# Optimization experiments

Hardware: AMD Instinct MI355X
Metric: run time of the kernel (lower is better)

The kernel has to match this reference:

```python
import jax, jax.numpy as jnp
import numpy as np

MAX_ITERS = 256  # matches init_kwargs max_iters


def setup_inputs() -> dict:
    key = jax.random.key(0)
    k1, k2 = jax.random.split(key)
    H = W = 4096
    # classic Mandelbrot viewing window
    c_real = jax.random.uniform(k1, (H, W), jnp.float32, -2.0, 0.5)
    c_imag = jax.random.uniform(k2, (H, W), jnp.float32, -1.25, 1.25)
    return {"c_real": c_real, "c_imag": c_imag}


def reference(c_real, c_imag):
    # z starts at c (NOT zero), as in the torch module
    zr0 = c_real
    zi0 = c_imag
    active0 = jnp.ones(c_real.shape, dtype=bool)
    counts0 = jnp.full(c_real.shape, float(MAX_ITERS), dtype=c_real.dtype)

    def body(step, state):
        zr, zi, active, counts = state
        escaped_now = active & (zr * zr + zi * zi >= 4.0)
        counts = jnp.where(escaped_now, step.astype(counts.dtype), counts)
        active = active & ~escaped_now
        # torch loop only updates z for step < max_iters
        do_update = active & (step < MAX_ITERS)
        next_real = zr * zr - zi * zi + c_real
        next_imag = 2.0 * zr * zi + c_imag
        zr = jnp.where(do_update, next_real, zr)
        zi = jnp.where(do_update, next_imag, zi)
        return (zr, zi, active, counts)

    _, _, _, counts = jax.lax.fori_loop(
        0, MAX_ITERS + 1, body, (zr0, zi0, active0, counts0)
    )
    return counts
```

## Files before the change

kernel.cpp:

```cpp
#include <hip/hip_runtime.h>


#define MAX_ITERS 256

__device__ __forceinline__ float mul32(float a, float b) {
    float d; asm("v_mul_f32 %0, %1, %2" : "=v"(d) : "v"(a), "v"(b)); return d;
}
__device__ __forceinline__ float add32(float a, float b) {
    float d; asm("v_add_f32 %0, %1, %2" : "=v"(d) : "v"(a), "v"(b)); return d;
}
__device__ __forceinline__ float fma32(float a, float b, float c) {
    float d; asm("v_fma_f32 %0, %1, %2, %3" : "=v"(d) : "v"(a), "v"(b), "v"(c)); return d;
}
__device__ __forceinline__ float fma32_negc(float a, float b, float c) {
    float d; asm("v_fma_f32 %0, %1, %2, -%3" : "=v"(d) : "v"(a), "v"(b), "v"(c)); return d;
}

__device__ __forceinline__ void iter_checks(float cr, float ci,
                                            float& zr, float& zi,
                                            float& act, float& cnt, int nchecks)
{
    #pragma unroll 8
    for (int s = 0; s < nchecks; ++s) {
        const float zi2 = mul32(zi, zi);
        const float mag = fma32(zr, zr, zi2);
        act = (mag < 4.0f) ? act : 0.0f;
        cnt = cnt + act;
        const float t   = fma32_negc(zr, zr, zi2);
        const float nr  = add32(t, cr);
        const float t2  = add32(zr, zr);
        zi = fma32(t2, zi, ci);
        zr = nr;
    }
}

__global__ void zero_ctrs(unsigned char* ws) {
    if (threadIdx.x < 64) *(unsigned*)(ws + (size_t)threadIdx.x * 64u) = 0u;
}

__global__ __launch_bounds__(256) void mandel_stage_a(
    const float* __restrict__ c_real, const float* __restrict__ c_imag,
    float* __restrict__ out, unsigned char* __restrict__ ws,
    unsigned seg_cap, int n)
{
    int i = blockIdx.x * blockDim.x + threadIdx.x;
    if (i >= n) return;
    const float cr = c_real[i];
    const float ci = c_imag[i];

    const float xq = cr - 0.25f;
    const float q  = xq * xq + ci * ci;
    const bool in_card = (q * (q + xq) - 0.25f * ci * ci) < -1e-3f;
    const float xb = cr + 1.0f;
    const bool in_bulb = (xb * xb + ci * ci) < (0.0625f - 1e-3f);
    const bool shortcut = in_card | in_bulb;

    float zr = cr, zi = ci, act = 1.0f, cnt = 0.0f;
    iter_checks(cr, ci, zr, zi, act, cnt, 16);

    const bool surv = (!shortcut) && (act != 0.0f);

    const unsigned long long m = __ballot(surv);
    if (m != 0ull) {
        const int lane = __builtin_amdgcn_mbcnt_hi(
            ~0u, __builtin_amdgcn_mbcnt_lo(~0u, 0));
        const int leader = (int)__ffsll((unsigned long long)m) - 1;
        const int seg = blockIdx.x & 63;
        unsigned* ctr = (unsigned*)(ws + (size_t)seg * 64u);
        unsigned base = 0u;
        if (lane == leader) base = atomicAdd(ctr, (unsigned)__popcll(m));
        base = (unsigned)__shfl((int)base, leader, 64);
        if (surv) {
            const unsigned rank = (unsigned)__popcll(m & ((1ull << lane) - 1ull));
            const unsigned slot = base + rank;
            if (slot < seg_cap) {
                float4* q1 = (float4*)(ws + 4096);
                int*    q2 = (int*)(ws + 4096 + (size_t)seg_cap * 64u * 16u);
                const size_t p = (size_t)seg * seg_cap + slot;
                q1[p] = make_float4(zr, zi, cr, ci);
                q2[p] = i;
                return;
            }
            iter_checks(cr, ci, zr, zi, act, cnt, 240);
            out[i] = cnt;
            return;
        }
    }
    out[i] = shortcut ? 256.0f : cnt;
}

__global__ __launch_bounds__(256) void mandel_stage_b(
    float* __restrict__ out, const unsigned char* __restrict__ ws,
    unsigned seg_cap, int blocks_per_seg)
{
    const int seg = (int)(blockIdx.x & 63u);
    const int grp = (int)(blockIdx.x >> 6);
    const unsigned cnt_s = *(const unsigned*)(ws + (size_t)seg * 64u);
    const unsigned nq = (cnt_s < seg_cap) ? cnt_s : seg_cap;
    const float4* q1 = (const float4*)(ws + 4096);
    const int*    q2 = (const int*)(ws + 4096 + (size_t)seg_cap * 64u * 16u);
    const unsigned stride = (unsigned)blocks_per_seg * 256u;
    for (unsigned j = (unsigned)grp * 256u + threadIdx.x; j < nq; j += stride) {
        const size_t p = (size_t)seg * seg_cap + j;
        const float4 rec = q1[p];
        const int idx = q2[p];
        float zr = rec.x, zi = rec.y;
        const float cr = rec.z, ci = rec.w;
        float act = 1.0f, cnt = 16.0f;
        iter_checks(cr, ci, zr, zi, act, cnt, 240);
        out[idx] = cnt;
    }
}

__global__ __launch_bounds__(256) void mandel_mono(
    const float* __restrict__ c_real, const float* __restrict__ c_imag,
    float* __restrict__ out, int n)
{
    int i = blockIdx.x * blockDim.x + threadIdx.x;
    if (i >= n) return;
    const float cr = c_real[i], ci = c_imag[i];
    float zr = cr, zi = ci, act = 1.0f, cnt = 0.0f;
    iter_checks(cr, ci, zr, zi, act, cnt, MAX_ITERS);
    out[i] = cnt;
}

extern "C" void kernel_launch(void* const* d_in, const int* in_sizes, int n_in,
                              void* d_out, int out_size, void* d_ws, size_t ws_size,
                              hipStream_t stream)
{
    const float* c_real = (const float*)d_in[0];
    const float* c_imag = (const float*)d_in[1];
    float* out = (float*)d_out;
    const int n = in_sizes[0];
    const int block = 256;
    const int gridA = (n + block - 1) / block;

    unsigned char* ws = (unsigned char*)d_ws;
    const size_t avail = (ws_size > 4096) ? (ws_size - 4096) : 0;
    unsigned seg_cap = (unsigned)(avail / (64u * 20u));

    if (seg_cap < 1024u) {
        mandel_mono<<<gridA, block, 0, stream>>>(c_real, c_imag, out, n);
        return;
    }

    zero_ctrs<<<1, 64, 0, stream>>>(ws);
    mandel_stage_a<<<gridA, block, 0, stream>>>(c_real, c_imag, out, ws,
                                                seg_cap, n);
    const int blocks_per_seg = 256;
    mandel_stage_b<<<64 * blocks_per_seg, block, 0, stream>>>(out, ws, seg_cap,
                                                              blocks_per_seg);
}
```

Measured before the change: 258.3 us.

## Make stage B persistent with per-lane dynamic refill from segment queues

Stage B changes from a static grid-stride loop, where each thread runs a full 240-iteration check, to a persistent kernel. Each lane works in 12-iteration chunks and, once its pixel escapes or finishes, grabs a new queued pixel through a wave-level atomic cursor per segment. The goal is to cut SIMD divergence waste, where lanes whose pixels escaped early sat idle while slower lanes in the same wavefront finished. In exchange it adds per-chunk ballots, atomics and scattered queue loads, and launches far fewer blocks. The counter-zeroing kernel now also clears the new cursor words.

```diff
diff --git a/kernel.cpp b/kernel.cpp
--- a/kernel.cpp
+++ b/kernel.cpp
@@ -35,7 +35,9 @@
 }
 
 __global__ void zero_ctrs(unsigned char* ws) {
-    if (threadIdx.x < 64) *(unsigned*)(ws + (size_t)threadIdx.x * 64u) = 0u;
+    if (threadIdx.x < 128)
+        *(unsigned*)(ws + (size_t)(threadIdx.x >> 1) * 64u
+                        + (size_t)(threadIdx.x & 1) * 4u) = 0u;
 }
 
 __global__ __launch_bounds__(256) void mandel_stage_a(
@@ -90,25 +92,53 @@
 }
 
 __global__ __launch_bounds__(256) void mandel_stage_b(
-    float* __restrict__ out, const unsigned char* __restrict__ ws,
-    unsigned seg_cap, int blocks_per_seg)
+    float* __restrict__ out, unsigned char* __restrict__ ws,
+    unsigned seg_cap)
 {
     const int seg = (int)(blockIdx.x & 63u);
-    const int grp = (int)(blockIdx.x >> 6);
     const unsigned cnt_s = *(const unsigned*)(ws + (size_t)seg * 64u);
     const unsigned nq = (cnt_s < seg_cap) ? cnt_s : seg_cap;
     const float4* q1 = (const float4*)(ws + 4096);
     const int*    q2 = (const int*)(ws + 4096 + (size_t)seg_cap * 64u * 16u);
-    const unsigned stride = (unsigned)blocks_per_seg * 256u;
-    for (unsigned j = (unsigned)grp * 256u + threadIdx.x; j < nq; j += stride) {
-        const size_t p = (size_t)seg * seg_cap + j;
-        const float4 rec = q1[p];
-        const int idx = q2[p];
-        float zr = rec.x, zi = rec.y;
-        const float cr = rec.z, ci = rec.w;
-        float act = 1.0f, cnt = 16.0f;
-        iter_checks(cr, ci, zr, zi, act, cnt, 240);
-        out[idx] = cnt;
+    unsigned* cursor = (unsigned*)(ws + (size_t)seg * 64u + 4u);
+
+    const int lane = __builtin_amdgcn_mbcnt_hi(
+        ~0u, __builtin_amdgcn_mbcnt_lo(~0u, 0));
+
+    float zr = 0.0f, zi = 0.0f, cr = 0.0f, ci = 0.0f, act = 0.0f, cnt = 0.0f;
+    int idx = 0, done = 0;
+    bool have = false;
+    bool q_empty = (nq == 0u);
+
+    for (;;) {
+        if (have && (act == 0.0f || done >= 240)) {
+            out[idx] = cnt;
+            have = false;
+        }
+        const unsigned long long need_m = __ballot(!have);
+        if (!q_empty && need_m != 0ull) {
+            const int leader = (int)__ffsll(need_m) - 1;
+            unsigned base = 0u;
+            if (lane == leader)
+                base = atomicAdd(cursor, (unsigned)__popcll(need_m));
+            base = (unsigned)__shfl((int)base, leader, 64);
+            if (base >= nq) q_empty = true;
+            if (!have) {
+                const unsigned slot = base +
+                    (unsigned)__popcll(need_m & ((1ull << lane) - 1ull));
+                if (slot < nq) {
+                    const size_t p = (size_t)seg * seg_cap + slot;
+                    const float4 rec = q1[p];
+                    idx = q2[p];
+                    zr = rec.x; zi = rec.y; cr = rec.z; ci = rec.w;
+                    act = 1.0f; cnt = 16.0f; done = 0;
+                    have = true;
+                }
+            }
+        }
+        if (__ballot(have) == 0ull) break;
+        iter_checks(cr, ci, zr, zi, act, cnt, 12);
+        done += 12;
     }
 }
 
@@ -144,10 +174,8 @@
         return;
     }
 
-    zero_ctrs<<<1, 64, 0, stream>>>(ws);
+    zero_ctrs<<<1, 128, 0, stream>>>(ws);
     mandel_stage_a<<<gridA, block, 0, stream>>>(c_real, c_imag, out, ws,
                                                 seg_cap, n);
-    const int blocks_per_seg = 256;
-    mandel_stage_b<<<64 * blocks_per_seg, block, 0, stream>>>(out, ws, seg_cap,
-                                                              blocks_per_seg);
+    mandel_stage_b<<<64 * 32, block, 0, stream>>>(out, ws, seg_cap);
 }
```

After: 277.0 us. 7.2% more time.

## Add multi-stage compaction pipeline with ping-pong queues for escaping points

Applied to the files above, without the earlier changes.

Replaces the single second stage with a chain of three strip kernels (40, 80, 120 iterations) that re-compact surviving points into alternating ping-pong queues using wave ballot and atomic counters. This cuts wasted lanes spent on points that escape early in the long tail, improving SIMD utilization. It costs extra kernel launches, extra queue reads and writes, and more atomics. The path is used only when the workspace is large enough for two queues, otherwise the old two-stage path runs.

```diff
diff --git a/kernel.cpp b/kernel.cpp
--- a/kernel.cpp
+++ b/kernel.cpp
@@ -34,8 +34,14 @@
     }
 }
 
+__device__ __forceinline__ int lane_id() {
+    return __builtin_amdgcn_mbcnt_hi(~0u, __builtin_amdgcn_mbcnt_lo(~0u, 0));
+}
+
 __global__ void zero_ctrs(unsigned char* ws) {
-    if (threadIdx.x < 64) *(unsigned*)(ws + (size_t)threadIdx.x * 64u) = 0u;
+    if (threadIdx.x < 256)
+        *(unsigned*)(ws + (size_t)(threadIdx.x >> 2) * 64u
+                        + (size_t)(threadIdx.x & 3) * 4u) = 0u;
 }
 
 __global__ __launch_bounds__(256) void mandel_stage_a(
@@ -62,8 +68,7 @@
 
     const unsigned long long m = __ballot(surv);
     if (m != 0ull) {
-        const int lane = __builtin_amdgcn_mbcnt_hi(
-            ~0u, __builtin_amdgcn_mbcnt_lo(~0u, 0));
+        const int lane = lane_id();
         const int leader = (int)__ffsll((unsigned long long)m) - 1;
         const int seg = blockIdx.x & 63;
         unsigned* ctr = (unsigned*)(ws + (size_t)seg * 64u);
@@ -74,11 +79,11 @@
             const unsigned rank = (unsigned)__popcll(m & ((1ull << lane) - 1ull));
             const unsigned slot = base + rank;
             if (slot < seg_cap) {
-                float4* q1 = (float4*)(ws + 4096);
-                int*    q2 = (int*)(ws + 4096 + (size_t)seg_cap * 64u * 16u);
+                float4* q1f = (float4*)(ws + 4096);
+                int*    q1i = (int*)(ws + 4096 + (size_t)seg_cap * 64u * 16u);
                 const size_t p = (size_t)seg * seg_cap + slot;
-                q1[p] = make_float4(zr, zi, cr, ci);
-                q2[p] = i;
+                q1f[p] = make_float4(zr, zi, cr, ci);
+                q1i[p] = i;
                 return;
             }
             iter_checks(cr, ci, zr, zi, act, cnt, 240);
@@ -89,7 +94,64 @@
     out[i] = shortcut ? 256.0f : cnt;
 }
 
-__global__ __launch_bounds__(256) void mandel_stage_b(
+template <int NCHECKS, int START, bool HAS_DST>
+__global__ __launch_bounds__(256) void mandel_strip(
+    float* __restrict__ out, unsigned char* __restrict__ ws,
+    const float4* __restrict__ srcF, const int* __restrict__ srcI,
+    float4* __restrict__ dstF, int* __restrict__ dstI,
+    int src_ctr, int dst_ctr, unsigned seg_cap, int blocks_per_seg)
+{
+    const int seg = (int)(blockIdx.x & 63u);
+    const int grp = (int)(blockIdx.x >> 6);
+    const unsigned cnt_s = *(const unsigned*)(ws + (size_t)seg * 64u
+                                                 + (size_t)src_ctr * 4u);
+    const unsigned nq = (cnt_s < seg_cap) ? cnt_s : seg_cap;
+    const unsigned stride = (unsigned)blocks_per_seg * 256u;
+    const int lane = lane_id();
+
+    for (unsigned j = (unsigned)grp * 256u + threadIdx.x; j < nq; j += stride) {
+        const size_t p = (size_t)seg * seg_cap + j;
+        const float4 rec = srcF[p];
+        const int idx = srcI[p];
+        float zr = rec.x, zi = rec.y;
+        const float cr = rec.z, ci = rec.w;
+        float act = 1.0f, cnt = (float)START;
+        iter_checks(cr, ci, zr, zi, act, cnt, NCHECKS);
+
+        if (HAS_DST) {
+            const bool surv = (act != 0.0f);
+            const unsigned long long m = __ballot(surv);
+            if (m != 0ull) {
+                const int leader = (int)__ffsll((unsigned long long)m) - 1;
+                unsigned* ctr = (unsigned*)(ws + (size_t)seg * 64u
+                                               + (size_t)dst_ctr * 4u);
+                unsigned base = 0u;
+                if (lane == leader) base = atomicAdd(ctr, (unsigned)__popcll(m));
+                base = (unsigned)__shfl((int)base, leader, 64);
+                if (surv) {
+                    const unsigned rank =
+                        (unsigned)__popcll(m & ((1ull << lane) - 1ull));
+                    const unsigned slot = base + rank;
+                    if (slot < seg_cap) {
+                        const size_t sp = (size_t)seg * seg_cap + slot;
+                        dstF[sp] = make_float4(zr, zi, cr, ci);
+                        dstI[sp] = idx;
+                        continue;
+                    }
+                    iter_checks(cr, ci, zr, zi, act, cnt,
+                                256 - START - NCHECKS);
+                    out[idx] = cnt;
+                    continue;
+                }
+            }
+            out[idx] = cnt;
+        } else {
+            out[idx] = cnt;
+        }
+    }
+}
+
+__global__ __launch_bounds__(256) void mandel_stage_b_fixed(
     float* __restrict__ out, const unsigned char* __restrict__ ws,
     unsigned seg_cap, int blocks_per_seg)
 {
@@ -97,13 +159,13 @@
     const int grp = (int)(blockIdx.x >> 6);
     const unsigned cnt_s = *(const unsigned*)(ws + (size_t)seg * 64u);
     const unsigned nq = (cnt_s < seg_cap) ? cnt_s : seg_cap;
-    const float4* q1 = (const float4*)(ws + 4096);
-    const int*    q2 = (const int*)(ws + 4096 + (size_t)seg_cap * 64u * 16u);
+    const float4* q1f = (const float4*)(ws + 4096);
+    const int*    q1i = (const int*)(ws + 4096 + (size_t)seg_cap * 64u * 16u);
     const unsigned stride = (unsigned)blocks_per_seg * 256u;
     for (unsigned j = (unsigned)grp * 256u + threadIdx.x; j < nq; j += stride) {
         const size_t p = (size_t)seg * seg_cap + j;
-        const float4 rec = q1[p];
-        const int idx = q2[p];
+        const float4 rec = q1f[p];
+        const int idx = q1i[p];
         float zr = rec.x, zi = rec.y;
         const float cr = rec.z, ci = rec.w;
         float act = 1.0f, cnt = 16.0f;
@@ -137,17 +199,38 @@
 
     unsigned char* ws = (unsigned char*)d_ws;
     const size_t avail = (ws_size > 4096) ? (ws_size - 4096) : 0;
-    unsigned seg_cap = (unsigned)(avail / (64u * 20u));
-
-    if (seg_cap < 1024u) {
+    const unsigned seg_cap1 = (unsigned)(avail / (64u * 20u));
+    const unsigned seg_cap2 = (unsigned)(avail / (64u * 20u * 2u));
+
+    if (seg_cap1 < 1024u) {
         mandel_mono<<<gridA, block, 0, stream>>>(c_real, c_imag, out, n);
         return;
     }
 
-    zero_ctrs<<<1, 64, 0, stream>>>(ws);
+    zero_ctrs<<<1, 256, 0, stream>>>(ws);
+
+    if (seg_cap2 >= 33000u) {
+        const unsigned sc = seg_cap2;
+        float4* q0f = (float4*)(ws + 4096);
+        int*    q0i = (int*)(ws + 4096 + (size_t)sc * 64u * 16u);
+        float4* q1f = (float4*)(ws + 4096 + (size_t)sc * 64u * 20u);
+        int*    q1i = (int*)(ws + 4096 + (size_t)sc * 64u * 20u
+                                       + (size_t)sc * 64u * 16u);
+
+        mandel_stage_a<<<gridA, block, 0, stream>>>(c_real, c_imag, out, ws,
+                                                    sc, n);
+        mandel_strip<40, 16, true><<<64 * 128, block, 0, stream>>>(
+            out, ws, q0f, q0i, q1f, q1i, 0, 1, sc, 128);
+        mandel_strip<80, 56, true><<<64 * 64, block, 0, stream>>>(
+            out, ws, q1f, q1i, q0f, q0i, 1, 2, sc, 64);
+        mandel_strip<120, 136, false><<<64 * 64, block, 0, stream>>>(
+            out, ws, q0f, q0i, (float4*)nullptr, (int*)nullptr, 2, 0, sc, 64);
+        return;
+    }
+
     mandel_stage_a<<<gridA, block, 0, stream>>>(c_real, c_imag, out, ws,
-                                                seg_cap, n);
+                                                seg_cap1, n);
     const int blocks_per_seg = 256;
-    mandel_stage_b<<<64 * blocks_per_seg, block, 0, stream>>>(out, ws, seg_cap,
-                                                              blocks_per_seg);
-}
+    mandel_stage_b_fixed<<<64 * blocks_per_seg, block, 0, stream>>>(
+        out, ws, seg_cap1, blocks_per_seg);
+}
```

Measured after the change: 252.6 us. -2.2%, faster.

## Process two points per thread using packed FP32 instructions in both stages

Applied to the files above, without the earlier changes.

Rewrites stage A and stage B so each thread iterates two Mandelbrot points together with v_pk_mul/v_pk_fma/v_pk_add packed FP32 instructions. The goal is to halve the per-point VALU instruction count of the escape loop. Stage B pairs queue entries k and k+half and uses fewer blocks per segment, while the fallback threshold for seg_cap is raised. The cost is more register pressure, lower thread-level parallelism, and extra divergence, because the two points in a pair can escape at different iterations.

```diff
diff --git a/kernel.cpp b/kernel.cpp
--- a/kernel.cpp
+++ b/kernel.cpp
@@ -2,6 +2,8 @@
 
 
 #define MAX_ITERS 256
+
+typedef __attribute__((ext_vector_type(2))) float f32x2;
 
 __device__ __forceinline__ float mul32(float a, float b) {
     float d; asm("v_mul_f32 %0, %1, %2" : "=v"(d) : "v"(a), "v"(b)); return d;
@@ -34,62 +36,132 @@
     }
 }
 
-__global__ void zero_ctrs(unsigned char* ws) {
-    if (threadIdx.x < 64) *(unsigned*)(ws + (size_t)threadIdx.x * 64u) = 0u;
-}
-
-__global__ __launch_bounds__(256) void mandel_stage_a(
-    const float* __restrict__ c_real, const float* __restrict__ c_imag,
-    float* __restrict__ out, unsigned char* __restrict__ ws,
-    unsigned seg_cap, int n)
-{
-    int i = blockIdx.x * blockDim.x + threadIdx.x;
-    if (i >= n) return;
-    const float cr = c_real[i];
-    const float ci = c_imag[i];
-
+__device__ __forceinline__ void check_pk(const f32x2 cr, const f32x2 ci,
+                                         f32x2& zr, f32x2& zi,
+                                         float& act0, float& act1,
+                                         float& cnt0, float& cnt1)
+{
+    f32x2 zi2, mag, t, t2;
+    asm("v_pk_mul_f32 %0, %2, %2\n\t"
+        "v_pk_fma_f32 %1, %3, %3, %0"
+        : "=&v"(zi2), "=&v"(mag)
+        : "v"(zi), "v"(zr));
+    const f32x2 mzi2 = -zi2;
+    asm("v_pk_fma_f32 %0, %2, %2, %4\n\t"
+        "v_pk_add_f32 %1, %2, %2\n\t"
+        "v_pk_add_f32 %2, %0, %5\n\t"
+        "v_pk_fma_f32 %3, %1, %3, %6"
+        : "=&v"(t), "=&v"(t2), "+v"(zr), "+v"(zi)
+        : "v"(mzi2), "v"(cr), "v"(ci));
+    act0 = (mag.x < 4.0f) ? act0 : 0.0f;
+    act1 = (mag.y < 4.0f) ? act1 : 0.0f;
+    cnt0 += act0;
+    cnt1 += act1;
+}
+
+__device__ __forceinline__ void iter_checks_pk(const f32x2 cr, const f32x2 ci,
+                                               f32x2& zr, f32x2& zi,
+                                               float& act0, float& act1,
+                                               float& cnt0, float& cnt1,
+                                               int nchecks)
+{
+    #pragma unroll 8
+    for (int s = 0; s < nchecks; ++s)
+        check_pk(cr, ci, zr, zi, act0, act1, cnt0, cnt1);
+}
+
+__device__ __forceinline__ int lane_id() {
+    return __builtin_amdgcn_mbcnt_hi(~0u, __builtin_amdgcn_mbcnt_lo(~0u, 0));
+}
+
+__device__ __forceinline__ bool in_shortcut(float cr, float ci) {
     const float xq = cr - 0.25f;
     const float q  = xq * xq + ci * ci;
     const bool in_card = (q * (q + xq) - 0.25f * ci * ci) < -1e-3f;
     const float xb = cr + 1.0f;
     const bool in_bulb = (xb * xb + ci * ci) < (0.0625f - 1e-3f);
-    const bool shortcut = in_card | in_bulb;
-
-    float zr = cr, zi = ci, act = 1.0f, cnt = 0.0f;
-    iter_checks(cr, ci, zr, zi, act, cnt, 16);
-
-    const bool surv = (!shortcut) && (act != 0.0f);
-
-    const unsigned long long m = __ballot(surv);
-    if (m != 0ull) {
-        const int lane = __builtin_amdgcn_mbcnt_hi(
-            ~0u, __builtin_amdgcn_mbcnt_lo(~0u, 0));
-        const int leader = (int)__ffsll((unsigned long long)m) - 1;
+    return in_card | in_bulb;
+}
+
+__global__ void zero_ctrs(unsigned char* ws) {
+    if (threadIdx.x < 64)
+        *(unsigned*)(ws + (size_t)threadIdx.x * 64u) = 0u;
+}
+
+__global__ __launch_bounds__(256) void mandel_stage_a_pk(
+    const float* __restrict__ c_real, const float* __restrict__ c_imag,
+    float* __restrict__ out, unsigned char* __restrict__ ws,
+    unsigned seg_cap, int n)
+{
+    const int tp = blockIdx.x * blockDim.x + threadIdx.x;
+    const int p0 = tp << 1;
+    if (p0 >= n) return;
+    const bool has1 = (p0 + 1) < n;
+
+    f32x2 cr, ci;
+    if (has1) {
+        cr = *(const f32x2*)(c_real + p0);
+        ci = *(const f32x2*)(c_imag + p0);
+    } else {
+        cr.x = c_real[p0]; cr.y = 0.0f;
+        ci.x = c_imag[p0]; ci.y = 0.0f;
+    }
+    const bool sc0 = in_shortcut(cr.x, ci.x);
+    const bool sc1 = in_shortcut(cr.y, ci.y);
+
+    f32x2 zr = cr, zi = ci;
+    float act0 = 1.0f, act1 = has1 ? 1.0f : 0.0f;
+    float cnt0 = 0.0f, cnt1 = 0.0f;
+    iter_checks_pk(cr, ci, zr, zi, act0, act1, cnt0, cnt1, 16);
+
+    const bool s0 = (!sc0) && (act0 != 0.0f);
+    const bool s1 = has1 && (!sc1) && (act1 != 0.0f);
+
+    const unsigned long long m0 = __ballot(s0);
+    const unsigned long long m1 = __ballot(s1);
+    if ((m0 | m1) != 0ull) {
+        const int lane = lane_id();
+        const int leader = (int)__ffsll(m0 | m1) - 1;
         const int seg = blockIdx.x & 63;
         unsigned* ctr = (unsigned*)(ws + (size_t)seg * 64u);
         unsigned base = 0u;
-        if (lane == leader) base = atomicAdd(ctr, (unsigned)__popcll(m));
+        if (lane == leader)
+            base = atomicAdd(ctr, (unsigned)(__popcll(m0) + __popcll(m1)));
         base = (unsigned)__shfl((int)base, leader, 64);
-        if (surv) {
-            const unsigned rank = (unsigned)__popcll(m & ((1ull << lane) - 1ull));
-            const unsigned slot = base + rank;
+        float4* qf = (float4*)(ws + 4096);
+        int*    qi = (int*)(ws + 4096 + (size_t)seg_cap * 64u * 16u);
+        if (s0) {
+            const unsigned slot = base +
+                (unsigned)__popcll(m0 & ((1ull << lane) - 1ull));
             if (slot < seg_cap) {
-                float4* q1 = (float4*)(ws + 4096);
-                int*    q2 = (int*)(ws + 4096 + (size_t)seg_cap * 64u * 16u);
                 const size_t p = (size_t)seg * seg_cap + slot;
-                q1[p] = make_float4(zr, zi, cr, ci);
-                q2[p] = i;
-                return;
+                qf[p] = make_float4(zr.x, zi.x, cr.x, ci.x);
+                qi[p] = p0;
+            } else {
+                float zrs = zr.x, zis = zi.x, as = 1.0f, cs = cnt0;
+                iter_checks(cr.x, ci.x, zrs, zis, as, cs, 240);
+                out[p0] = cs;
             }
-            iter_checks(cr, ci, zr, zi, act, cnt, 240);
-            out[i] = cnt;
-            return;
         }
-    }
-    out[i] = shortcut ? 256.0f : cnt;
-}
-
-__global__ __launch_bounds__(256) void mandel_stage_b(
+        if (s1) {
+            const unsigned slot = base + (unsigned)__popcll(m0) +
+                (unsigned)__popcll(m1 & ((1ull << lane) - 1ull));
+            if (slot < seg_cap) {
+                const size_t p = (size_t)seg * seg_cap + slot;
+                qf[p] = make_float4(zr.y, zi.y, cr.y, ci.y);
+                qi[p] = p0 + 1;
+            } else {
+                float zrs = zr.y, zis = zi.y, as = 1.0f, cs = cnt1;
+                iter_checks(cr.y, ci.y, zrs, zis, as, cs, 240);
+                out[p0 + 1] = cs;
+            }
+        }
+    }
+    if (!s0) out[p0] = sc0 ? 256.0f : cnt0;
+    if (has1 && !s1) out[p0 + 1] = sc1 ? 256.0f : cnt1;
+}
+
+__global__ __launch_bounds__(256) void mandel_stage_b_pk(
     float* __restrict__ out, const unsigned char* __restrict__ ws,
     unsigned seg_cap, int blocks_per_seg)
 {
@@ -97,18 +169,28 @@
     const int grp = (int)(blockIdx.x >> 6);
     const unsigned cnt_s = *(const unsigned*)(ws + (size_t)seg * 64u);
     const unsigned nq = (cnt_s < seg_cap) ? cnt_s : seg_cap;
-    const float4* q1 = (const float4*)(ws + 4096);
-    const int*    q2 = (const int*)(ws + 4096 + (size_t)seg_cap * 64u * 16u);
+    const unsigned half = (nq + 1u) >> 1;
     const unsigned stride = (unsigned)blocks_per_seg * 256u;
-    for (unsigned j = (unsigned)grp * 256u + threadIdx.x; j < nq; j += stride) {
-        const size_t p = (size_t)seg * seg_cap + j;
-        const float4 rec = q1[p];
-        const int idx = q2[p];
-        float zr = rec.x, zi = rec.y;
-        const float cr = rec.z, ci = rec.w;
-        float act = 1.0f, cnt = 16.0f;
-        iter_checks(cr, ci, zr, zi, act, cnt, 240);
-        out[idx] = cnt;
+    const float4* qf = (const float4*)(ws + 4096);
+    const int*    qi = (const int*)(ws + 4096 + (size_t)seg_cap * 64u * 16u);
+    const size_t segbase = (size_t)seg * seg_cap;
+
+    for (unsigned k = (unsigned)grp * 256u + threadIdx.x; k < half; k += stride) {
+        const unsigned r1 = k + half;
+        const bool v1 = (r1 < nq);
+        const float4 rec0 = qf[segbase + k];
+        const float4 rec1 = v1 ? qf[segbase + r1] : rec0;
+        const int idx0 = qi[segbase + k];
+        const int idx1 = v1 ? qi[segbase + r1] : -1;
+        f32x2 zr; zr.x = rec0.x; zr.y = rec1.x;
+        f32x2 zi; zi.x = rec0.y; zi.y = rec1.y;
+        f32x2 cr; cr.x = rec0.z; cr.y = rec1.z;
+        f32x2 ci; ci.x = rec0.w; ci.y = rec1.w;
+        float act0 = 1.0f, act1 = v1 ? 1.0f : 0.0f;
+        float cnt0 = 16.0f, cnt1 = 16.0f;
+        iter_checks_pk(cr, ci, zr, zi, act0, act1, cnt0, cnt1, 240);
+        out[idx0] = cnt0;
+        if (v1) out[idx1] = cnt1;
     }
 }
 
@@ -133,21 +215,23 @@
     float* out = (float*)d_out;
     const int n = in_sizes[0];
     const int block = 256;
-    const int gridA = (n + block - 1) / block;
 
     unsigned char* ws = (unsigned char*)d_ws;
     const size_t avail = (ws_size > 4096) ? (ws_size - 4096) : 0;
-    unsigned seg_cap = (unsigned)(avail / (64u * 20u));
-
-    if (seg_cap < 1024u) {
+    const unsigned seg_cap = (unsigned)(avail / (64u * 20u));
+
+    if (seg_cap < 8192u) {
+        const int gridA = (n + block - 1) / block;
         mandel_mono<<<gridA, block, 0, stream>>>(c_real, c_imag, out, n);
         return;
     }
 
     zero_ctrs<<<1, 64, 0, stream>>>(ws);
-    mandel_stage_a<<<gridA, block, 0, stream>>>(c_real, c_imag, out, ws,
-                                                seg_cap, n);
-    const int blocks_per_seg = 256;
-    mandel_stage_b<<<64 * blocks_per_seg, block, 0, stream>>>(out, ws, seg_cap,
-                                                              blocks_per_seg);
-}
+
+    const int npairs = (n + 1) / 2;
+    const int gridA = (npairs + block - 1) / block;
+    mandel_stage_a_pk<<<gridA, block, 0, stream>>>(c_real, c_imag, out,
+                                                   ws, seg_cap, n);
+    const int bps = 64;
+    mandel_stage_b_pk<<<64 * bps, block, 0, stream>>>(out, ws, seg_cap, bps);
+}
```

Measured after the change: 240.4 us. 6.9% less time.
